# Optimization experiments

Measured on AMD Instinct MI355X. Metric: run time of the kernel, lower is better.

Reference implementation:

```python
import jax, jax.numpy as jnp
import numpy as np

N, E, F = 20000, 320000, 128
H = 2 * F  # MLP width = 256
EPS = 1e-5
TANH_ALPHA = 1.0


def setup_inputs() -> dict:
    key = jax.random.key(0)
    ks = jax.random.split(key, 16)
    x = jax.random.normal(ks[0], (N, F), dtype=jnp.float32)
    edge_index = jax.random.randint(ks[1], (2, E), 0, N, dtype=jnp.int64)
    s = 1.0 / np.sqrt(H)
    W1 = jax.random.uniform(ks[2], (H, H), jnp.float32, -s, s)
    b1 = jax.random.uniform(ks[3], (H,), jnp.float32, -s, s)
    g1 = jnp.ones((H,), jnp.float32)
    be1 = jnp.zeros((H,), jnp.float32)
    rm1 = jax.random.normal(ks[4], (H,), jnp.float32) * 0.1
    rv1 = jax.random.uniform(ks[5], (H,), jnp.float32, 0.5, 1.5)
    W2 = jax.random.uniform(ks[6], (H, H), jnp.float32, -s, s)
    b2 = jax.random.uniform(ks[7], (H,), jnp.float32, -s, s)
    g2 = jnp.ones((H,), jnp.float32)
    be2 = jnp.zeros((H,), jnp.float32)
    rm2 = jax.random.normal(ks[8], (H,), jnp.float32) * 0.1
    rv2 = jax.random.uniform(ks[9], (H,), jnp.float32, 0.5, 1.5)
    W3 = jax.random.uniform(ks[10], (F, H), jnp.float32, -s, s)
    b3 = jax.random.uniform(ks[11], (F,), jnp.float32, -s, s)
    return {"x": x, "edge_index": edge_index,
            "W1": W1, "b1": b1, "g1": g1, "be1": be1, "rm1": rm1, "rv1": rv1,
            "W2": W2, "b2": b2, "g2": g2, "be2": be2, "rm2": rm2, "rv2": rv2,
            "W3": W3, "b3": b3}


def _block(h, W, b, g, be, rm, rv):
    # Linear -> (Dropout inactive at eval) -> BatchNorm1d (eval, running stats) -> ReLU
    h = h @ W.T + b
    h = (h - rm) * (g * jax.lax.rsqrt(rv + EPS)) + be
    return jax.nn.relu(h)


def reference(x, edge_index, W1, b1, g1, be1, rm1, rv1,
              W2, b2, g2, be2, rm2, rv2, W3, b3):
    src, dst = edge_index[0], edge_index[1]  # PyG: x_j = x[src], x_i = x[dst]
    xi = x[dst]                              # [E, F]
    xj = x[src]                              # [E, F]
    h = jnp.concatenate([xi, xj - xi], axis=-1)  # [E, 2F]
    h = _block(h, W1, b1, g1, be1, rm1, rv1)
    h = _block(h, W2, b2, g2, be2, rm2, rv2)
    h = h @ W3.T + b3                        # [E, F]
    # scatter-mean aggregation over destination nodes
    summed = jax.ops.segment_sum(h, dst, num_segments=N)              # [N, F]
    cnt = jax.ops.segment_sum(jnp.ones((E,), h.dtype), dst, num_segments=N)
    agg = summed / jnp.maximum(cnt, 1.0)[:, None]
    return jnp.tanh(TANH_ALPHA * agg)
```

## Files before the change

kernel.cpp:

```cpp
#include <hip/hip_runtime.h>
#include <math.h>

#define NN 20000
#define EE 320000
#define FF 128
#define HH 256
#define HPITCH 264
#define TP3 132
#define MT 128

typedef __bf16   bf16x8 __attribute__((ext_vector_type(8)));
typedef __bf16   bf16x4 __attribute__((ext_vector_type(4)));
typedef _Float16 f16x8  __attribute__((ext_vector_type(8)));
typedef _Float16 f16x4  __attribute__((ext_vector_type(4)));
typedef float    f32x4  __attribute__((ext_vector_type(4)));

#define WPTR_OFF  80000
#define SPAIR_OFF 160000
#define XB_OFF    1440000
#define W2F_OFF   6560000
#define W3F_OFF   6691072
#define WCF_OFF   6756608
#define PQ_OFF    6887680

#define PB_XB   2500
#define PB_HIST 1250
#define PB_W2   32
#define PB_WC   32
#define PB_W3   16
#define PREP_BLOCKS (PB_XB + PB_HIST + PB_W2 + PB_WC + PB_W3)

#define NODEB 313


__global__ __launch_bounds__(256) void prep_kernel(
    const float* __restrict__ x,  const int* __restrict__ eidx,
    const float* __restrict__ W1, const float* __restrict__ W2,
    const float* __restrict__ W3,
    __bf16* __restrict__ xb, __bf16* __restrict__ w2f,
    __bf16* __restrict__ wcf, __bf16* __restrict__ w3f,
    int* __restrict__ cnt)
{
    const int b = blockIdx.x, t = threadIdx.x;
    if (b < PB_XB) {
        const size_t base = ((size_t)b * 256 + t) * 4;
        float4 v = *(const float4*)(x + base);
        __bf16 o[4] = {(__bf16)v.x, (__bf16)v.y, (__bf16)v.z, (__bf16)v.w};
        __builtin_memcpy(xb + base, o, 8);
    } else if (b < PB_XB + PB_HIST) {
        const int e = (b - PB_XB) * 256 + t;
        atomicAdd(&cnt[eidx[EE + e]], 1);
    } else if (b < PB_XB + PB_HIST + PB_W2) {
        const int f = (b - (PB_XB + PB_HIST)) * 256 + t;
        const int n = ((f >> 9) << 4) | (f & 15);
        const int k = (((f >> 6) & 7) << 5) | (((f >> 4) & 3) << 3);
        const float* s = W2 + (size_t)n * HH + k;
        __bf16 o[8];
        #pragma unroll
        for (int j = 0; j < 8; ++j) o[j] = (__bf16)s[j];
        __builtin_memcpy(w2f + (size_t)f * 8, o, 16);
    } else if (b < PB_XB + PB_HIST + PB_W2 + PB_WC) {
        const int f = (b - (PB_XB + PB_HIST + PB_W2)) * 256 + t;
        const int n = ((f >> 8) << 4) | (f & 15);
        const int k = (((f >> 6) & 3) << 5) | (((f >> 4) & 3) << 3);
        __bf16 o[8];
        if (n < HH) {
            const float* a = W1 + (size_t)n * HH + k;
            #pragma unroll
            for (int j = 0; j < 8; ++j) o[j] = (__bf16)(a[j] - a[FF + j]);
        } else {
            const float* a = W1 + (size_t)(n - HH) * HH + FF + k;
            #pragma unroll
            for (int j = 0; j < 8; ++j) o[j] = (__bf16)a[j];
        }
        __builtin_memcpy(wcf + (size_t)f * 8, o, 16);
    } else {
        const int f = (b - (PB_XB + PB_HIST + PB_W2 + PB_WC)) * 256 + t;
        const int n = ((f >> 9) << 4) | (f & 15);
        const int k = (((f >> 6) & 7) << 5) | (((f >> 4) & 3) << 3);
        const float* s = W3 + (size_t)n * HH + k;
        __bf16 o[8];
        #pragma unroll
        for (int j = 0; j < 8; ++j) o[j] = (__bf16)s[j];
        __builtin_memcpy(w3f + (size_t)f * 8, o, 16);
    }
}

__global__ __launch_bounds__(512) void node_kernel(
    const __bf16* __restrict__ xb, const __bf16* __restrict__ wcf,
    const float* __restrict__ b1, const float* __restrict__ g1,
    const float* __restrict__ be1, const float* __restrict__ rm1,
    const float* __restrict__ rv1,
    _Float16* __restrict__ PQ,
    const int* __restrict__ cnt, int* __restrict__ wptr)
{
    if (blockIdx.x == NODEB) {
        __shared__ int sp[512];
        const int t = threadIdx.x;
        const int base = t * 40;
        int s = 0;
        #pragma unroll 1
        for (int i = 0; i < 40; ++i) { const int idx = base + i; if (idx < NN) s += cnt[idx]; }
        sp[t] = s;
        __syncthreads();
        for (int d = 1; d < 512; d <<= 1) {
            const int v = (t >= d) ? sp[t - d] : 0;
            __syncthreads();
            sp[t] += v;
            __syncthreads();
        }
        int run = sp[t] - s;
        #pragma unroll 1
        for (int i = 0; i < 40; ++i) {
            const int idx = base + i;
            if (idx < NN) { wptr[idx] = run; run += cnt[idx]; }
        }
        return;
    }

    const int tid = threadIdx.x;
    const int lane = tid & 63, wv = tid >> 6;
    const int lr = lane & 15, lq = lane >> 4;
    const int node0 = blockIdx.x * 64;

    f32x4 acc[4][4];
    #pragma unroll
    for (int i = 0; i < 4; ++i)
        #pragma unroll
        for (int j = 0; j < 4; ++j) acc[i][j] = (f32x4){0.f, 0.f, 0.f, 0.f};

    const bf16x8* wb = (const bf16x8*)wcf + (size_t)(wv * 16) * 64 + lane;
    #pragma unroll 1
    for (int kb = 0; kb < 4; ++kb) {
        bf16x8 wf[4], af[4];
        #pragma unroll
        for (int j = 0; j < 4; ++j) wf[j] = wb[(j * 4 + kb) * 64];
        #pragma unroll
        for (int i = 0; i < 4; ++i) {
            int nd = node0 + i * 16 + lr;
            if (nd > NN - 1) nd = NN - 1;
            af[i] = *(const bf16x8*)(xb + (size_t)nd * FF + kb * 32 + lq * 8);
        }
        #pragma unroll
        for (int i = 0; i < 4; ++i)
            #pragma unroll
            for (int j = 0; j < 4; ++j)
                acc[i][j] = __builtin_amdgcn_mfma_f32_16x16x32_bf16(wf[j], af[i], acc[i][j], 0, 0, 0);
    }

    #pragma unroll
    for (int j = 0; j < 4; ++j) {
        const int n0 = wv * 64 + j * 16 + lq * 4;
        const int ch = (n0 < HH) ? n0 : n0 - HH;
        float sc[4], cc[4];
        #pragma unroll
        for (int r = 0; r < 4; ++r) {
            const float s1 = g1[ch + r] * rsqrtf(rv1[ch + r] + 1e-5f);
            sc[r] = s1;
            cc[r] = (n0 < HH) ? (b1[ch + r] - rm1[ch + r]) * s1 + be1[ch + r] : 0.f;
        }
        #pragma unroll
        for (int i = 0; i < 4; ++i) {
            const int nd = node0 + i * 16 + lr;
            if (nd < NN) {
                f16x4 o;
                #pragma unroll
                for (int r = 0; r < 4; ++r) o[r] = (_Float16)(acc[i][j][r] * sc[r] + cc[r]);
                *(f16x4*)(PQ + (size_t)nd * 512 + n0) = o;
            }
        }
    }
}

__global__ __launch_bounds__(256) void scatter_kernel(const int* __restrict__ eidx,
                                                      int* __restrict__ wptr,
                                                      unsigned int* __restrict__ spair)
{
    const int e = blockIdx.x * 256 + threadIdx.x;
    if (e < EE) {
        const int d = eidx[EE + e];
        const int pos = atomicAdd(&wptr[d], 1);
        spair[pos] = (unsigned int)eidx[e] | ((unsigned int)d << 16);
    }
}

__global__ __launch_bounds__(512, 4) void fused_edge_mlp(
    const _Float16* __restrict__ PQ,
    const unsigned int* __restrict__ spair,
    const __bf16* __restrict__ W2f,
    const float* __restrict__ b2, const float* __restrict__ g2,
    const float* __restrict__ be2, const float* __restrict__ rm2,
    const float* __restrict__ rv2,
    const __bf16* __restrict__ W3f,
    float* __restrict__ outp)
{
    __shared__ __align__(16) __bf16 sh_h[MT * HPITCH];
    __shared__ __align__(16) float s_scale[HH];
    __shared__ __align__(16) float s_c[HH];
    __shared__ int s_dst[MT];
    __shared__ int s_src[MT];

    const int tid = threadIdx.x;
    const int xcd = blockIdx.x & 7, bi = blockIdx.x >> 3;
    const int swz = (xcd < 4) ? (xcd * 313 + bi) : (1252 + (xcd - 4) * 312 + bi);
    const int e0 = swz * MT;

    if (tid < MT) {
        const unsigned int v = spair[e0 + tid];
        s_src[tid] = (int)(v & 0xffffu);
        s_dst[tid] = (int)(v >> 16);
    }
    if (tid < HH) {
        const float sc = g2[tid] * rsqrtf(rv2[tid] + 1e-5f);
        s_scale[tid] = sc;
        s_c[tid] = (b2[tid] - rm2[tid]) * sc + be2[tid];
    }
    __syncthreads();

    {
        const int r = tid >> 2, q = tid & 3;
        const f16x8* pd = (const f16x8*)(PQ + (size_t)s_dst[r] * 512 + q * 64);
        const f16x8* ps = (const f16x8*)(PQ + (size_t)s_src[r] * 512 + 256 + q * 64);
        bf16x8* hr = (bf16x8*)&sh_h[r * HPITCH + q * 64];
        #pragma unroll
        for (int i = 0; i < 8; ++i) {
            const f16x8 a = pd[i];
            const f16x8 bq = ps[i];
            bf16x8 o;
            #pragma unroll
            for (int j = 0; j < 8; ++j)
                o[j] = (__bf16)fmaxf((float)a[j] + (float)bq[j], 0.f);
            hr[i] = o;
        }
    }
    __syncthreads();

    const int lane = tid & 63, wv = tid >> 6;
    const int lr = lane & 15, lq = lane >> 4;

    {
        const int wm = wv >> 2, wn = wv & 3;
        const int m_base = wm * 64;
        f32x4 acc[4][4];
        #pragma unroll
        for (int i = 0; i < 4; ++i)
            #pragma unroll
            for (int j = 0; j < 4; ++j) acc[i][j] = (f32x4){0.f, 0.f, 0.f, 0.f};

        const bf16x8* wb = (const bf16x8*)W2f + (size_t)(wn * 4) * 8 * 64 + lane;
        #pragma unroll 1
        for (int kb = 0; kb < 8; ++kb) {
            bf16x8 wf[4], af[4];
            #pragma unroll
            for (int j = 0; j < 4; ++j) wf[j] = wb[(j * 8 + kb) * 64];
            #pragma unroll
            for (int i = 0; i < 4; ++i)
                af[i] = *(const bf16x8*)&sh_h[(m_base + i * 16 + lr) * HPITCH + kb * 32 + lq * 8];
            #pragma unroll
            for (int i = 0; i < 4; ++i)
                #pragma unroll
                for (int j = 0; j < 4; ++j)
                    acc[i][j] = __builtin_amdgcn_mfma_f32_16x16x32_bf16(wf[j], af[i], acc[i][j], 0, 0, 0);
        }
        __syncthreads();
        #pragma unroll
        for (int j = 0; j < 4; ++j) {
            const int n0 = wn * 64 + j * 16 + lq * 4;
            const float4 sc4 = *(const float4*)&s_scale[n0];
            const float4 cc4 = *(const float4*)&s_c[n0];
            #pragma unroll
            for (int i = 0; i < 4; ++i) {
                const int m = m_base + i * 16 + lr;
                bf16x4 o;
                o[0] = (__bf16)fmaxf(acc[i][j][0] * sc4.x + cc4.x, 0.f);
                o[1] = (__bf16)fmaxf(acc[i][j][1] * sc4.y + cc4.y, 0.f);
                o[2] = (__bf16)fmaxf(acc[i][j][2] * sc4.z + cc4.z, 0.f);
                o[3] = (__bf16)fmaxf(acc[i][j][3] * sc4.w + cc4.w, 0.f);
                *(bf16x4*)&sh_h[m * HPITCH + n0] = o;
            }
        }
        __syncthreads();
    }

    {
        const int wm = wv >> 1, wn = wv & 1;
        const int m_base = wm * 32;
        f32x4 acc[2][4];
        #pragma unroll
        for (int i = 0; i < 2; ++i)
            #pragma unroll
            for (int j = 0; j < 4; ++j) acc[i][j] = (f32x4){0.f, 0.f, 0.f, 0.f};

        const bf16x8* wb = (const bf16x8*)W3f + (size_t)(wn * 4) * 8 * 64 + lane;
        #pragma unroll 1
        for (int kb = 0; kb < 8; ++kb) {
            bf16x8 wf[4], af[2];
            #pragma unroll
            for (int j = 0; j < 4; ++j) wf[j] = wb[(j * 8 + kb) * 64];
            #pragma unroll
            for (int i = 0; i < 2; ++i)
                af[i] = *(const bf16x8*)&sh_h[(m_base + i * 16 + lr) * HPITCH + kb * 32 + lq * 8];
            #pragma unroll
            for (int i = 0; i < 2; ++i)
                #pragma unroll
                for (int j = 0; j < 4; ++j)
                    acc[i][j] = __builtin_amdgcn_mfma_f32_16x16x32_bf16(wf[j], af[i], acc[i][j], 0, 0, 0);
        }
        __syncthreads();
        float* tile = (float*)sh_h;
        #pragma unroll
        for (int j = 0; j < 4; ++j) {
            const int n0 = wn * 64 + j * 16 + lq * 4;
            #pragma unroll
            for (int i = 0; i < 2; ++i) {
                const int m = m_base + i * 16 + lr;
                *(f32x4*)&tile[m * TP3 + n0] = acc[i][j];
            }
        }
        __syncthreads();

        {
            const int col = tid & 127;
            const int r0 = (tid >> 7) * 32;
            int cur = s_dst[r0];
            float run = 0.f;
            #pragma unroll 1
            for (int r = r0; r < r0 + 32; ++r) {
                const int d = s_dst[r];
                if (d != cur) {
                    atomicAdd(&outp[(size_t)cur * FF + col], run);
                    run = 0.f; cur = d;
                }
                run += tile[r * TP3 + col];
            }
            atomicAdd(&outp[(size_t)cur * FF + col], run);
        }
    }
}

__global__ __launch_bounds__(256) void finalize_kernel(const int* __restrict__ cnt,
                                                       const float* __restrict__ b3,
                                                       float* __restrict__ out)
{
    const int i = blockIdx.x * 256 + threadIdx.x;
    if (i < NN * FF) {
        const float c = fmaxf((float)cnt[i >> 7], 1.0f);
        out[i] = tanhf(out[i] / c + b3[i & 127]);
    }
}

extern "C" void kernel_launch(void* const* d_in, const int* in_sizes, int n_in,
                              void* d_out, int out_size, void* d_ws, size_t ws_size,
                              hipStream_t stream)
{
    const float* x   = (const float*)d_in[0];
    const int*   ei  = (const int*)d_in[1];
    const float* W1  = (const float*)d_in[2];
    const float* b1  = (const float*)d_in[3];
    const float* g1  = (const float*)d_in[4];
    const float* be1 = (const float*)d_in[5];
    const float* rm1 = (const float*)d_in[6];
    const float* rv1 = (const float*)d_in[7];
    const float* W2  = (const float*)d_in[8];
    const float* b2  = (const float*)d_in[9];
    const float* g2  = (const float*)d_in[10];
    const float* be2 = (const float*)d_in[11];
    const float* rm2 = (const float*)d_in[12];
    const float* rv2 = (const float*)d_in[13];
    const float* W3  = (const float*)d_in[14];
    const float* b3  = (const float*)d_in[15];

    char* ws = (char*)d_ws;
    int* cnt_i = (int*)ws;
    int* wptr  = (int*)(ws + WPTR_OFF);
    unsigned int* spair = (unsigned int*)(ws + SPAIR_OFF);
    __bf16* xb  = (__bf16*)(ws + XB_OFF);
    __bf16* w2f = (__bf16*)(ws + W2F_OFF);
    __bf16* w3f = (__bf16*)(ws + W3F_OFF);
    __bf16* wcf = (__bf16*)(ws + WCF_OFF);
    _Float16* PQ = (_Float16*)(ws + PQ_OFF);
    float* outp = (float*)d_out;

    hipMemsetAsync(cnt_i, 0, NN * sizeof(int), stream);
    hipMemsetAsync(d_out, 0, (size_t)NN * FF * sizeof(float), stream);

    prep_kernel<<<PREP_BLOCKS, 256, 0, stream>>>(x, ei, W1, W2, W3,
                                                 xb, w2f, wcf, w3f, cnt_i);
    node_kernel<<<NODEB + 1, 512, 0, stream>>>(xb, wcf, b1, g1, be1, rm1, rv1,
                                               PQ, cnt_i, wptr);
    scatter_kernel<<<(EE + 255) / 256, 256, 0, stream>>>(ei, wptr, spair);
    fused_edge_mlp<<<EE / MT, 512, 0, stream>>>(PQ, spair,
                                                w2f, b2, g2, be2, rm2, rv2,
                                                w3f, outp);
    finalize_kernel<<<(NN * FF + 255) / 256, 256, 0, stream>>>(cnt_i, b3, outp);
}
```

Baseline: 297.0 us.

## Switch edge MLP to fp16, repartition GEMM waves, prefetch gathers, vectorize finalize

Converts all staged operands and MFMA calls from bf16 to fp16, so the gathered fp16 PQ rows are summed and ReLU'd in packed half arithmetic without float conversion. The layer-2 and layer-3 GEMMs are repartitioned so each wave owns a narrow N slice over all 128 rows, with weight fragments software-prefetched one k-step ahead. The PQ gathers are issued before the shared index and BN setup, which removes one barrier. The finalize kernel processes four elements per thread with a reciprocal multiply. fp16 narrows the dynamic range, which could overflow on unusual inputs.

```diff
diff --git a/kernel.cpp b/kernel.cpp
--- a/kernel.cpp
+++ b/kernel.cpp
@@ -9,26 +9,24 @@
 #define TP3 132
 #define MT 128
 
-typedef __bf16   bf16x8 __attribute__((ext_vector_type(8)));
-typedef __bf16   bf16x4 __attribute__((ext_vector_type(4)));
-typedef _Float16 f16x8  __attribute__((ext_vector_type(8)));
-typedef _Float16 f16x4  __attribute__((ext_vector_type(4)));
-typedef float    f32x4  __attribute__((ext_vector_type(4)));
+typedef _Float16 f16x8 __attribute__((ext_vector_type(8)));
+typedef _Float16 f16x4 __attribute__((ext_vector_type(4)));
+typedef float    f32x4 __attribute__((ext_vector_type(4)));
 
 #define WPTR_OFF  80000
 #define SPAIR_OFF 160000
-#define XB_OFF    1440000
+#define XH_OFF    1440000
 #define W2F_OFF   6560000
 #define W3F_OFF   6691072
 #define WCF_OFF   6756608
 #define PQ_OFF    6887680
 
-#define PB_XB   2500
+#define PB_XH   2500
 #define PB_HIST 1250
 #define PB_W2   32
 #define PB_WC   32
 #define PB_W3   16
-#define PREP_BLOCKS (PB_XB + PB_HIST + PB_W2 + PB_WC + PB_W3)
+#define PREP_BLOCKS (PB_XH + PB_HIST + PB_W2 + PB_WC + PB_W3)
 
 #define NODEB 313
 
@@ -37,57 +35,57 @@
     const float* __restrict__ x,  const int* __restrict__ eidx,
     const float* __restrict__ W1, const float* __restrict__ W2,
     const float* __restrict__ W3,
-    __bf16* __restrict__ xb, __bf16* __restrict__ w2f,
-    __bf16* __restrict__ wcf, __bf16* __restrict__ w3f,
+    _Float16* __restrict__ xh, _Float16* __restrict__ w2f,
+    _Float16* __restrict__ wcf, _Float16* __restrict__ w3f,
     int* __restrict__ cnt)
 {
     const int b = blockIdx.x, t = threadIdx.x;
-    if (b < PB_XB) {
+    if (b < PB_XH) {
         const size_t base = ((size_t)b * 256 + t) * 4;
         float4 v = *(const float4*)(x + base);
-        __bf16 o[4] = {(__bf16)v.x, (__bf16)v.y, (__bf16)v.z, (__bf16)v.w};
-        __builtin_memcpy(xb + base, o, 8);
-    } else if (b < PB_XB + PB_HIST) {
-        const int e = (b - PB_XB) * 256 + t;
+        _Float16 o[4] = {(_Float16)v.x, (_Float16)v.y, (_Float16)v.z, (_Float16)v.w};
+        __builtin_memcpy(xh + base, o, 8);
+    } else if (b < PB_XH + PB_HIST) {
+        const int e = (b - PB_XH) * 256 + t;
         atomicAdd(&cnt[eidx[EE + e]], 1);
-    } else if (b < PB_XB + PB_HIST + PB_W2) {
-        const int f = (b - (PB_XB + PB_HIST)) * 256 + t;
+    } else if (b < PB_XH + PB_HIST + PB_W2) {
+        const int f = (b - (PB_XH + PB_HIST)) * 256 + t;
         const int n = ((f >> 9) << 4) | (f & 15);
         const int k = (((f >> 6) & 7) << 5) | (((f >> 4) & 3) << 3);
         const float* s = W2 + (size_t)n * HH + k;
-        __bf16 o[8];
-        #pragma unroll
-        for (int j = 0; j < 8; ++j) o[j] = (__bf16)s[j];
+        _Float16 o[8];
+        #pragma unroll
+        for (int j = 0; j < 8; ++j) o[j] = (_Float16)s[j];
         __builtin_memcpy(w2f + (size_t)f * 8, o, 16);
-    } else if (b < PB_XB + PB_HIST + PB_W2 + PB_WC) {
-        const int f = (b - (PB_XB + PB_HIST + PB_W2)) * 256 + t;
+    } else if (b < PB_XH + PB_HIST + PB_W2 + PB_WC) {
+        const int f = (b - (PB_XH + PB_HIST + PB_W2)) * 256 + t;
         const int n = ((f >> 8) << 4) | (f & 15);
         const int k = (((f >> 6) & 3) << 5) | (((f >> 4) & 3) << 3);
-        __bf16 o[8];
+        _Float16 o[8];
         if (n < HH) {
             const float* a = W1 + (size_t)n * HH + k;
             #pragma unroll
-            for (int j = 0; j < 8; ++j) o[j] = (__bf16)(a[j] - a[FF + j]);
+            for (int j = 0; j < 8; ++j) o[j] = (_Float16)(a[j] - a[FF + j]);
         } else {
             const float* a = W1 + (size_t)(n - HH) * HH + FF + k;
             #pragma unroll
-            for (int j = 0; j < 8; ++j) o[j] = (__bf16)a[j];
+            for (int j = 0; j < 8; ++j) o[j] = (_Float16)a[j];
         }
         __builtin_memcpy(wcf + (size_t)f * 8, o, 16);
     } else {
-        const int f = (b - (PB_XB + PB_HIST + PB_W2 + PB_WC)) * 256 + t;
+        const int f = (b - (PB_XH + PB_HIST + PB_W2 + PB_WC)) * 256 + t;
         const int n = ((f >> 9) << 4) | (f & 15);
         const int k = (((f >> 6) & 7) << 5) | (((f >> 4) & 3) << 3);
         const float* s = W3 + (size_t)n * HH + k;
-        __bf16 o[8];
-        #pragma unroll
-        for (int j = 0; j < 8; ++j) o[j] = (__bf16)s[j];
+        _Float16 o[8];
+        #pragma unroll
+        for (int j = 0; j < 8; ++j) o[j] = (_Float16)s[j];
         __builtin_memcpy(w3f + (size_t)f * 8, o, 16);
     }
 }
 
 __global__ __launch_bounds__(512) void node_kernel(
-    const __bf16* __restrict__ xb, const __bf16* __restrict__ wcf,
+    const _Float16* __restrict__ xh, const _Float16* __restrict__ wcf,
     const float* __restrict__ b1, const float* __restrict__ g1,
     const float* __restrict__ be1, const float* __restrict__ rm1,
     const float* __restrict__ rv1,
@@ -129,23 +127,23 @@
         #pragma unroll
         for (int j = 0; j < 4; ++j) acc[i][j] = (f32x4){0.f, 0.f, 0.f, 0.f};
 
-    const bf16x8* wb = (const bf16x8*)wcf + (size_t)(wv * 16) * 64 + lane;
+    const f16x8* wb = (const f16x8*)wcf + (size_t)(wv * 16) * 64 + lane;
     #pragma unroll 1
     for (int kb = 0; kb < 4; ++kb) {
-        bf16x8 wf[4], af[4];
+        f16x8 wf[4], af[4];
         #pragma unroll
         for (int j = 0; j < 4; ++j) wf[j] = wb[(j * 4 + kb) * 64];
         #pragma unroll
         for (int i = 0; i < 4; ++i) {
             int nd = node0 + i * 16 + lr;
             if (nd > NN - 1) nd = NN - 1;
-            af[i] = *(const bf16x8*)(xb + (size_t)nd * FF + kb * 32 + lq * 8);
+            af[i] = *(const f16x8*)(xh + (size_t)nd * FF + kb * 32 + lq * 8);
         }
         #pragma unroll
         for (int i = 0; i < 4; ++i)
             #pragma unroll
             for (int j = 0; j < 4; ++j)
-                acc[i][j] = __builtin_amdgcn_mfma_f32_16x16x32_bf16(wf[j], af[i], acc[i][j], 0, 0, 0);
+                acc[i][j] = __builtin_amdgcn_mfma_f32_16x16x32_f16(wf[j], af[i], acc[i][j], 0, 0, 0);
     }
 
     #pragma unroll
@@ -187,49 +185,52 @@
 __global__ __launch_bounds__(512, 4) void fused_edge_mlp(
     const _Float16* __restrict__ PQ,
     const unsigned int* __restrict__ spair,
-    const __bf16* __restrict__ W2f,
+    const _Float16* __restrict__ W2f,
     const float* __restrict__ b2, const float* __restrict__ g2,
     const float* __restrict__ be2, const float* __restrict__ rm2,
     const float* __restrict__ rv2,
-    const __bf16* __restrict__ W3f,
+    const _Float16* __restrict__ W3f,
     float* __restrict__ outp)
 {
-    __shared__ __align__(16) __bf16 sh_h[MT * HPITCH];
+    __shared__ __align__(16) _Float16 sh_h[MT * HPITCH];
     __shared__ __align__(16) float s_scale[HH];
     __shared__ __align__(16) float s_c[HH];
     __shared__ int s_dst[MT];
-    __shared__ int s_src[MT];
 
     const int tid = threadIdx.x;
     const int xcd = blockIdx.x & 7, bi = blockIdx.x >> 3;
     const int swz = (xcd < 4) ? (xcd * 313 + bi) : (1252 + (xcd - 4) * 312 + bi);
     const int e0 = swz * MT;
 
-    if (tid < MT) {
-        const unsigned int v = spair[e0 + tid];
-        s_src[tid] = (int)(v & 0xffffu);
-        s_dst[tid] = (int)(v >> 16);
-    }
-    if (tid < HH) {
-        const float sc = g2[tid] * rsqrtf(rv2[tid] + 1e-5f);
-        s_scale[tid] = sc;
-        s_c[tid] = (b2[tid] - rm2[tid]) * sc + be2[tid];
-    }
-    __syncthreads();
-
     {
         const int r = tid >> 2, q = tid & 3;
-        const f16x8* pd = (const f16x8*)(PQ + (size_t)s_dst[r] * 512 + q * 64);
-        const f16x8* ps = (const f16x8*)(PQ + (size_t)s_src[r] * 512 + 256 + q * 64);
-        bf16x8* hr = (bf16x8*)&sh_h[r * HPITCH + q * 64];
+        const unsigned int pv = spair[e0 + r];
+        const int dr = (int)(pv >> 16), sr = (int)(pv & 0xffffu);
+        const f16x8* pd = (const f16x8*)(PQ + (size_t)dr * 512 + q * 64);
+        const f16x8* ps = (const f16x8*)(PQ + (size_t)sr * 512 + 256 + q * 64);
+        f16x8 av[8], bv[8];
+        #pragma unroll
+        for (int i = 0; i < 8; ++i) av[i] = pd[i];
+        #pragma unroll
+        for (int i = 0; i < 8; ++i) bv[i] = ps[i];
+
+        if (tid < MT) s_dst[tid] = (int)(spair[e0 + tid] >> 16);
+        if (tid < HH) {
+            const float sc = g2[tid] * rsqrtf(rv2[tid] + 1e-5f);
+            s_scale[tid] = sc;
+            s_c[tid] = (b2[tid] - rm2[tid]) * sc + be2[tid];
+        }
+
+        f16x8* hr = (f16x8*)&sh_h[r * HPITCH + q * 64];
         #pragma unroll
         for (int i = 0; i < 8; ++i) {
-            const f16x8 a = pd[i];
-            const f16x8 bq = ps[i];
-            bf16x8 o;
-            #pragma unroll
-            for (int j = 0; j < 8; ++j)
-                o[j] = (__bf16)fmaxf((float)a[j] + (float)bq[j], 0.f);
+            f16x8 s = av[i] + bv[i];
+            f16x8 o;
+            #pragma unroll
+            for (int j = 0; j < 8; ++j) {
+                const _Float16 z = (_Float16)0;
+                o[j] = s[j] > z ? s[j] : z;
+            }
             hr[i] = o;
         }
     }
@@ -239,84 +240,81 @@
     const int lr = lane & 15, lq = lane >> 4;
 
     {
-        const int wm = wv >> 2, wn = wv & 3;
-        const int m_base = wm * 64;
-        f32x4 acc[4][4];
-        #pragma unroll
-        for (int i = 0; i < 4; ++i)
-            #pragma unroll
-            for (int j = 0; j < 4; ++j) acc[i][j] = (f32x4){0.f, 0.f, 0.f, 0.f};
-
-        const bf16x8* wb = (const bf16x8*)W2f + (size_t)(wn * 4) * 8 * 64 + lane;
+        f32x4 acc[8][2];
+        #pragma unroll
+        for (int i = 0; i < 8; ++i) { acc[i][0] = (f32x4){0.f,0.f,0.f,0.f}; acc[i][1] = (f32x4){0.f,0.f,0.f,0.f}; }
+
+        const int nt0 = wv * 2;
+        const f16x8* wbase = (const f16x8*)W2f + lane;
+        f16x8 cw0 = wbase[(nt0 * 8) * 64];
+        f16x8 cw1 = wbase[((nt0 + 1) * 8) * 64];
         #pragma unroll 1
         for (int kb = 0; kb < 8; ++kb) {
-            bf16x8 wf[4], af[4];
-            #pragma unroll
-            for (int j = 0; j < 4; ++j) wf[j] = wb[(j * 8 + kb) * 64];
-            #pragma unroll
-            for (int i = 0; i < 4; ++i)
-                af[i] = *(const bf16x8*)&sh_h[(m_base + i * 16 + lr) * HPITCH + kb * 32 + lq * 8];
-            #pragma unroll
-            for (int i = 0; i < 4; ++i)
+            f16x8 nw0 = wbase[(nt0 * 8 + kb + 1) * 64];
+            f16x8 nw1 = wbase[((nt0 + 1) * 8 + kb + 1) * 64];
+            #pragma unroll
+            for (int h = 0; h < 2; ++h) {
+                f16x8 af[4];
                 #pragma unroll
-                for (int j = 0; j < 4; ++j)
-                    acc[i][j] = __builtin_amdgcn_mfma_f32_16x16x32_bf16(wf[j], af[i], acc[i][j], 0, 0, 0);
+                for (int i = 0; i < 4; ++i)
+                    af[i] = *(const f16x8*)&sh_h[((h * 4 + i) * 16 + lr) * HPITCH + kb * 32 + lq * 8];
+                #pragma unroll
+                for (int i = 0; i < 4; ++i) {
+                    acc[h*4+i][0] = __builtin_amdgcn_mfma_f32_16x16x32_f16(cw0, af[i], acc[h*4+i][0], 0, 0, 0);
+                    acc[h*4+i][1] = __builtin_amdgcn_mfma_f32_16x16x32_f16(cw1, af[i], acc[h*4+i][1], 0, 0, 0);
+                }
+            }
+            cw0 = nw0; cw1 = nw1;
         }
         __syncthreads();
         #pragma unroll
-        for (int j = 0; j < 4; ++j) {
-            const int n0 = wn * 64 + j * 16 + lq * 4;
+        for (int j = 0; j < 2; ++j) {
+            const int n0 = (nt0 + j) * 16 + lq * 4;
             const float4 sc4 = *(const float4*)&s_scale[n0];
             const float4 cc4 = *(const float4*)&s_c[n0];
             #pragma unroll
-            for (int i = 0; i < 4; ++i) {
-                const int m = m_base + i * 16 + lr;
-                bf16x4 o;
-                o[0] = (__bf16)fmaxf(acc[i][j][0] * sc4.x + cc4.x, 0.f);
-                o[1] = (__bf16)fmaxf(acc[i][j][1] * sc4.y + cc4.y, 0.f);
-                o[2] = (__bf16)fmaxf(acc[i][j][2] * sc4.z + cc4.z, 0.f);
-                o[3] = (__bf16)fmaxf(acc[i][j][3] * sc4.w + cc4.w, 0.f);
-                *(bf16x4*)&sh_h[m * HPITCH + n0] = o;
+            for (int i = 0; i < 8; ++i) {
+                const int m = i * 16 + lr;
+                f16x4 o;
+                o[0] = (_Float16)fmaxf(acc[i][j][0] * sc4.x + cc4.x, 0.f);
+                o[1] = (_Float16)fmaxf(acc[i][j][1] * sc4.y + cc4.y, 0.f);
+                o[2] = (_Float16)fmaxf(acc[i][j][2] * sc4.z + cc4.z, 0.f);
+                o[3] = (_Float16)fmaxf(acc[i][j][3] * sc4.w + cc4.w, 0.f);
+                *(f16x4*)&sh_h[m * HPITCH + n0] = o;
             }
         }
         __syncthreads();
     }
 
     {
-        const int wm = wv >> 1, wn = wv & 1;
-        const int m_base = wm * 32;
-        f32x4 acc[2][4];
-        #pragma unroll
-        for (int i = 0; i < 2; ++i)
-            #pragma unroll
-            for (int j = 0; j < 4; ++j) acc[i][j] = (f32x4){0.f, 0.f, 0.f, 0.f};
-
-        const bf16x8* wb = (const bf16x8*)W3f + (size_t)(wn * 4) * 8 * 64 + lane;
+        f32x4 acc[8];
+        #pragma unroll
+        for (int i = 0; i < 8; ++i) acc[i] = (f32x4){0.f, 0.f, 0.f, 0.f};
+
+        const int nt = wv;
+        const f16x8* wbase = (const f16x8*)W3f + lane;
+        f16x8 cw = wbase[(nt * 8) * 64];
         #pragma unroll 1
         for (int kb = 0; kb < 8; ++kb) {
-            bf16x8 wf[4], af[2];
-            #pragma unroll
-            for (int j = 0; j < 4; ++j) wf[j] = wb[(j * 8 + kb) * 64];
-            #pragma unroll
-            for (int i = 0; i < 2; ++i)
-                af[i] = *(const bf16x8*)&sh_h[(m_base + i * 16 + lr) * HPITCH + kb * 32 + lq * 8];
-            #pragma unroll
-            for (int i = 0; i < 2; ++i)
+            f16x8 nw = wbase[(nt * 8 + kb + 1) * 64];
+            #pragma unroll
+            for (int h = 0; h < 2; ++h) {
+                f16x8 af[4];
                 #pragma unroll
-                for (int j = 0; j < 4; ++j)
-                    acc[i][j] = __builtin_amdgcn_mfma_f32_16x16x32_bf16(wf[j], af[i], acc[i][j], 0, 0, 0);
+                for (int i = 0; i < 4; ++i)
+                    af[i] = *(const f16x8*)&sh_h[((h * 4 + i) * 16 + lr) * HPITCH + kb * 32 + lq * 8];
+                #pragma unroll
+                for (int i = 0; i < 4; ++i)
+                    acc[h*4+i] = __builtin_amdgcn_mfma_f32_16x16x32_f16(cw, af[i], acc[h*4+i], 0, 0, 0);
+            }
+            cw = nw;
         }
         __syncthreads();
         float* tile = (float*)sh_h;
-        #pragma unroll
-        for (int j = 0; j < 4; ++j) {
-            const int n0 = wn * 64 + j * 16 + lq * 4;
-            #pragma unroll
-            for (int i = 0; i < 2; ++i) {
-                const int m = m_base + i * 16 + lr;
-                *(f32x4*)&tile[m * TP3 + n0] = acc[i][j];
-            }
-        }
+        const int n0 = nt * 16 + lq * 4;
+        #pragma unroll
+        for (int i = 0; i < 8; ++i)
+            *(f32x4*)&tile[(i * 16 + lr) * TP3 + n0] = acc[i];
         __syncthreads();
 
         {
@@ -342,10 +340,17 @@
                                                        const float* __restrict__ b3,
                                                        float* __restrict__ out)
 {
-    const int i = blockIdx.x * 256 + threadIdx.x;
-    if (i < NN * FF) {
-        const float c = fmaxf((float)cnt[i >> 7], 1.0f);
-        out[i] = tanhf(out[i] / c + b3[i & 127]);
+    const int i4 = (blockIdx.x * 256 + threadIdx.x) * 4;
+    if (i4 < NN * FF) {
+        const float c = fmaxf((float)cnt[i4 >> 7], 1.0f);
+        const float rc = 1.0f / c;
+        float4 v = *(const float4*)(out + i4);
+        const float* bb = b3 + (i4 & 127);
+        v.x = tanhf(v.x * rc + bb[0]);
+        v.y = tanhf(v.y * rc + bb[1]);
+        v.z = tanhf(v.z * rc + bb[2]);
+        v.w = tanhf(v.w * rc + bb[3]);
+        *(float4*)(out + i4) = v;
     }
 }
 
@@ -374,23 +379,23 @@
     int* cnt_i = (int*)ws;
     int* wptr  = (int*)(ws + WPTR_OFF);
     unsigned int* spair = (unsigned int*)(ws + SPAIR_OFF);
-    __bf16* xb  = (__bf16*)(ws + XB_OFF);
-    __bf16* w2f = (__bf16*)(ws + W2F_OFF);
-    __bf16* w3f = (__bf16*)(ws + W3F_OFF);
-    __bf16* wcf = (__bf16*)(ws + WCF_OFF);
-    _Float16* PQ = (_Float16*)(ws + PQ_OFF);
+    _Float16* xh  = (_Float16*)(ws + XH_OFF);
+    _Float16* w2f = (_Float16*)(ws + W2F_OFF);
+    _Float16* w3f = (_Float16*)(ws + W3F_OFF);
+    _Float16* wcf = (_Float16*)(ws + WCF_OFF);
+    _Float16* PQ  = (_Float16*)(ws + PQ_OFF);
     float* outp = (float*)d_out;
 
     hipMemsetAsync(cnt_i, 0, NN * sizeof(int), stream);
     hipMemsetAsync(d_out, 0, (size_t)NN * FF * sizeof(float), stream);
 
     prep_kernel<<<PREP_BLOCKS, 256, 0, stream>>>(x, ei, W1, W2, W3,
-                                                 xb, w2f, wcf, w3f, cnt_i);
-    node_kernel<<<NODEB + 1, 512, 0, stream>>>(xb, wcf, b1, g1, be1, rm1, rv1,
+                                                 xh, w2f, wcf, w3f, cnt_i);
+    node_kernel<<<NODEB + 1, 512, 0, stream>>>(xh, wcf, b1, g1, be1, rm1, rv1,
                                                PQ, cnt_i, wptr);
     scatter_kernel<<<(EE + 255) / 256, 256, 0, stream>>>(ei, wptr, spair);
     fused_edge_mlp<<<EE / MT, 512, 0, stream>>>(PQ, spair,
                                                 w2f, b2, g2, be2, rm2, rv2,
                                                 w3f, outp);
-    finalize_kernel<<<(NN * FF + 255) / 256, 256, 0, stream>>>(cnt_i, b3, outp);
-}
+    finalize_kernel<<<(NN * FF / 4 + 255) / 256, 256, 0, stream>>>(cnt_i, b3, outp);
+}
```

After: 286.7 us. -3.5%, faster.
